# Optimization experiments

Measured on AMD Instinct MI355X. Metric: run time of the kernel, lower is better.

Reference implementation:

```python
import jax, jax.numpy as jnp
import numpy as np

EMBED_DIM = 1024
NUM_HEADS = 16
HEAD_DIM = EMBED_DIM // NUM_HEADS
MLP_HIDDEN = 4096


def layer_norm(x, gamma, beta, eps=1e-5):
    mu = jnp.mean(x, axis=-1, keepdims=True)
    var = jnp.var(x, axis=-1, keepdims=True)
    return (x - mu) / jnp.sqrt(var + eps) * gamma + beta


def setup_inputs() -> dict:
    key = jax.random.key(0)
    ks = jax.random.split(key, 16)
    d, h = EMBED_DIM, MLP_HIDDEN
    s = 0.02
    inp = {
        "x": jax.random.normal(ks[0], (2, 2048, d), dtype=jnp.float32),
        "ln1_g": jnp.ones((d,), jnp.float32),
        "ln1_b": jnp.zeros((d,), jnp.float32),
        "ln2_g": jnp.ones((d,), jnp.float32),
        "ln2_b": jnp.zeros((d,), jnp.float32),
        "Wq": jax.random.normal(ks[1], (d, d), jnp.float32) * s,
        "bq": jnp.zeros((d,), jnp.float32),
        "Wk": jax.random.normal(ks[2], (d, d), jnp.float32) * s,
        "bk": jnp.zeros((d,), jnp.float32),
        "Wv": jax.random.normal(ks[3], (d, d), jnp.float32) * s,
        "bv": jnp.zeros((d,), jnp.float32),
        "Wo": jax.random.normal(ks[4], (d, d), jnp.float32) * s,
        "bo": jnp.zeros((d,), jnp.float32),
        "W1": jax.random.normal(ks[5], (d, h), jnp.float32) * s,
        "b1": jnp.zeros((h,), jnp.float32),
        "W2": jax.random.normal(ks[6], (h, d), jnp.float32) * s,
        "b2": jnp.zeros((d,), jnp.float32),
    }
    return inp


def reference(x, ln1_g, ln1_b, ln2_g, ln2_b, Wq, bq, Wk, bk, Wv, bv, Wo, bo, W1, b1, W2, b2):
    B, T, C = x.shape
    H, Dh = NUM_HEADS, HEAD_DIM
    # attention branch
    xn = layer_norm(x, ln1_g, ln1_b)
    q = (xn @ Wq + bq).reshape(B, T, H, Dh).transpose(0, 2, 1, 3)  # [B,H,T,Dh]
    k = (xn @ Wk + bk).reshape(B, T, H, Dh).transpose(0, 2, 1, 3)
    v = (xn @ Wv + bv).reshape(B, T, H, Dh).transpose(0, 2, 1, 3)
    scores = jnp.einsum('bhtd,bhsd->bhts', q, k) / jnp.sqrt(jnp.float32(Dh))
    attn = jax.nn.softmax(scores, axis=-1)
    out = jnp.einsum('bhts,bhsd->bhtd', attn, v)
    out = out.transpose(0, 2, 1, 3).reshape(B, T, C)
    x = x + out @ Wo + bo
    # MLP branch
    xn2 = layer_norm(x, ln2_g, ln2_b)
    x = x + jax.nn.relu(xn2 @ W1 + b1) @ W2 + b2
    return x
```

## Files before the change

### kernel.cpp

```cpp
#include <hip/hip_runtime.h>

typedef float f32x4 __attribute__((ext_vector_type(4)));
typedef __bf16 bf16x8 __attribute__((ext_vector_type(8)));

constexpr int TT   = 2048;
constexpr int CC   = 1024;
constexpr int HIDN = 4096;
constexpr int MM   = 4096;
constexpr int NQKV = 3072;

union U84 { uint32_t u[4]; bf16x8 v; };

__device__ inline uint32_t cvt_pk_bf16(float lo, float hi) {
  uint32_t r;
  asm("v_cvt_pk_bf16_f32 %0, %1, %2" : "=v"(r) : "v"(lo), "v"(hi));
  return r;
}
__device__ inline ushort f2bf(float f) { return (ushort)(cvt_pk_bf16(f, 0.f) & 0xffffu); }
__device__ inline float bfbits2f(uint32_t bits) {
  union { uint32_t u; float f; } c; c.u = bits; return c.f;
}
__device__ inline float exp2_fast(float x) {
  float r;
  asm("v_exp_f32 %0, %1" : "=v"(r) : "v"(x));
  return r;
}

#define AS1C(p) ((__attribute__((address_space(1))) void*)(p))
#define AS3(p)  ((__attribute__((address_space(3))) void*)(p))

__global__ __launch_bounds__(256) void prep_weights(const float* __restrict__ Wq,
                                                    const float* __restrict__ Wk,
                                                    const float* __restrict__ Wv,
                                                    const float* __restrict__ Wo,
                                                    const float* __restrict__ W1,
                                                    const float* __restrict__ W2,
                                                    const float* __restrict__ bq,
                                                    const float* __restrict__ bk,
                                                    const float* __restrict__ bv,
                                                    const float* __restrict__ x,
                                                    const float* __restrict__ g1,
                                                    const float* __restrict__ b1v,
                                                    ushort* __restrict__ WqkvT,
                                                    ushort* __restrict__ WoT,
                                                    ushort* __restrict__ W1T,
                                                    ushort* __restrict__ W2T,
                                                    float* __restrict__ Bqkv,
                                                    ushort* __restrict__ Xn) {
  const int id = blockIdx.x;
  const int t = threadIdx.x;
  if (id >= 12300) {
    const int row = id - 12300;
    float4 v = reinterpret_cast<const float4*>(x + (size_t)row * CC)[t];
    float s  = v.x + v.y + v.z + v.w;
    float ss = v.x * v.x + v.y * v.y + v.z * v.z + v.w * v.w;
#pragma unroll
    for (int off = 32; off; off >>= 1) {
      s  += __shfl_down(s, off);
      ss += __shfl_down(ss, off);
    }
    __shared__ float red[16];
    const int wid = t >> 6, lane = t & 63;
    if (lane == 0) { red[wid] = s; red[8 + wid] = ss; }
    __syncthreads();
    if (t == 0) {
      red[0] = red[0] + red[1] + red[2] + red[3];
      red[8] = red[8] + red[9] + red[10] + red[11];
    }
    __syncthreads();
    const float mu   = red[0] * (1.0f / CC);
    const float var  = red[8] * (1.0f / CC) - mu * mu;
    const float rstd = rsqrtf(var + 1e-5f);
    float4 gg = reinterpret_cast<const float4*>(g1)[t];
    float4 bb = reinterpret_cast<const float4*>(b1v)[t];
    uint2 st;
    st.x = cvt_pk_bf16((v.x - mu) * rstd * gg.x + bb.x, (v.y - mu) * rstd * gg.y + bb.y);
    st.y = cvt_pk_bf16((v.z - mu) * rstd * gg.z + bb.z, (v.w - mu) * rstd * gg.w + bb.w);
    *reinterpret_cast<uint2*>(Xn + (size_t)row * CC + t * 4) = st;
    return;
  }
  if (id >= 12288) {
    const int i = (id - 12288) * 256 + t;
    Bqkv[i] = (i < 1024) ? bq[i] : ((i < 2048) ? bk[i - 1024] : bv[i - 2048]);
    return;
  }
  const float* W; ushort* out; int Kd, Nd, bx, by, rowOff = 0;
  if (id < 4096) {
    const int which = id >> 10, sub = id & 1023;
    bx = sub & 31; by = sub >> 5; Kd = 1024; Nd = 1024;
    if (which == 0)      { W = Wq; out = WqkvT; rowOff = 0; }
    else if (which == 1) { W = Wk; out = WqkvT; rowOff = 1024; }
    else if (which == 2) { W = Wv; out = WqkvT; rowOff = 2048; }
    else                 { W = Wo; out = WoT; }
  } else if (id < 8192) {
    const int sub = id - 4096; bx = sub & 127; by = sub >> 7;
    W = W1; out = W1T; Kd = 1024; Nd = 4096;
  } else {
    const int sub = id - 8192; bx = sub & 31; by = sub >> 5;
    W = W2; out = W2T; Kd = 4096; Nd = 1024;
  }
  const int n0 = bx * 32, k0 = by * 32;
  __shared__ float Ts[32][33];
  {
    const int r = t >> 3, cb = (t & 7) * 4;
    float4 v = *reinterpret_cast<const float4*>(W + (size_t)(k0 + r) * Nd + n0 + cb);
    Ts[r][cb + 0] = v.x; Ts[r][cb + 1] = v.y; Ts[r][cb + 2] = v.z; Ts[r][cb + 3] = v.w;
  }
  __syncthreads();
  {
    const int nl = t >> 3, kb = (t & 7) * 4;
    uint2 st;
    st.x = cvt_pk_bf16(Ts[kb + 0][nl], Ts[kb + 1][nl]);
    st.y = cvt_pk_bf16(Ts[kb + 2][nl], Ts[kb + 3][nl]);
    *reinterpret_cast<uint2*>(out + (size_t)(rowOff + n0 + nl) * Kd + k0 + kb) = st;
  }
}

template <bool RELU, bool VOUT, bool PARTIAL>
__global__ __launch_bounds__(512, 2) void gemm_8w(const ushort* __restrict__ A,
                                                  const ushort* __restrict__ Bt,
                                                  const float* __restrict__ bias,
                                                  ushort* __restrict__ outp,
                                                  ushort* __restrict__ Vt,
                                                  ushort* __restrict__ P1,
                                                  ushort* __restrict__ P2,
                                                  ushort* __restrict__ P3,
                                                  int N, int K, int Kchunk) {
  __shared__ ushort lds[65536];
  const int t = threadIdx.x, lane = t & 63, w = t >> 6;
  const int g = lane >> 4, i16 = lane & 15;
  const int wr = w >> 2, wc = w & 3;
  const int nwg  = gridDim.x * gridDim.y;
  const int orig = blockIdx.y * gridDim.x + blockIdx.x;
  const int sw   = (orig & 7) * (nwg >> 3) + (orig >> 3);
  const int row0 = (sw / gridDim.x) * 256, col0 = (sw % gridDim.x) * 256;
  const int kstart = PARTIAL ? blockIdx.z * Kchunk : 0;
  const int NT = (PARTIAL ? Kchunk : K) >> 6;
  ushort* __restrict__ Out = outp;
  if (PARTIAL) Out = (blockIdx.z == 0) ? outp : (blockIdx.z == 1) ? P1
              : (blockIdx.z == 2) ? P2 : P3;

  const ushort* aG[4];
  const ushort* bG[4];
#pragma unroll
  for (int i = 0; i < 4; ++i) {
    const int c = t + 512 * i;
    const int r = c >> 3, ssw = (c & 7) ^ (r & 7);
    aG[i] = A  + (size_t)(row0 + r) * K + kstart + ssw * 8;
    bG[i] = Bt + (size_t)(col0 + r) * K + kstart + ssw * 8;
  }

  int aoff[8][2], boff[4][2];
#pragma unroll
  for (int mf = 0; mf < 8; ++mf) {
    const int R = wr * 128 + mf * 16 + i16;
#pragma unroll
    for (int kk = 0; kk < 2; ++kk)
      aoff[mf][kk] = R * 128 + (((kk << 2) | g) ^ (R & 7)) * 16;
  }
#pragma unroll
  for (int nf = 0; nf < 4; ++nf) {
    const int Cn = wc * 64 + nf * 16 + i16;
#pragma unroll
    for (int kk = 0; kk < 2; ++kk)
      boff[nf][kk] = Cn * 128 + (((kk << 2) | g) ^ (Cn & 7)) * 16;
  }

  f32x4 acc[8][4] = {};

  auto STAGE = [&](int bi, int kt) {
    char* aB = (char*)lds + bi * 65536;
    char* bB = aB + 32768;
    const int ko = kt * 64;
#pragma unroll
    for (int i = 0; i < 4; ++i)
      __builtin_amdgcn_global_load_lds(AS1C(aG[i] + ko), AS3(aB + i * 8192 + w * 1024), 16, 0, 0);
#pragma unroll
    for (int i = 0; i < 4; ++i)
      __builtin_amdgcn_global_load_lds(AS1C(bG[i] + ko), AS3(bB + i * 8192 + w * 1024), 16, 0, 0);
  };

  STAGE(0, 0);

  for (int kt = 0; kt < NT; ++kt) {
    const int cur = kt & 1;
    if (kt + 1 < NT) {
      STAGE(cur ^ 1, kt + 1);
      asm volatile("s_waitcnt vmcnt(8)" ::: "memory");
    } else {
      asm volatile("s_waitcnt vmcnt(0)" ::: "memory");
    }
    asm volatile("s_barrier" ::: "memory");
    __builtin_amdgcn_sched_barrier(0);

    const char* aB = (const char*)lds + cur * 65536;
    const char* bB = aB + 32768;
    bf16x8 b4[4][2], a4[4][2];
#pragma unroll
    for (int nf = 0; nf < 4; ++nf)
#pragma unroll
      for (int kk = 0; kk < 2; ++kk)
        b4[nf][kk] = *reinterpret_cast<const bf16x8*>(bB + boff[nf][kk]);
#pragma unroll
    for (int mf = 0; mf < 4; ++mf)
#pragma unroll
      for (int kk = 0; kk < 2; ++kk)
        a4[mf][kk] = *reinterpret_cast<const bf16x8*>(aB + aoff[mf][kk]);
    __builtin_amdgcn_s_setprio(1);
#pragma unroll
    for (int mf = 0; mf < 4; ++mf)
#pragma unroll
      for (int nf = 0; nf < 4; ++nf)
#pragma unroll
        for (int kk = 0; kk < 2; ++kk)
          acc[mf][nf] = __builtin_amdgcn_mfma_f32_16x16x32_bf16(a4[mf][kk], b4[nf][kk], acc[mf][nf], 0, 0, 0);
    __builtin_amdgcn_s_setprio(0);
    asm volatile("s_barrier" ::: "memory");
    __builtin_amdgcn_sched_barrier(0);
#pragma unroll
    for (int mf = 0; mf < 4; ++mf)
#pragma unroll
      for (int kk = 0; kk < 2; ++kk)
        a4[mf][kk] = *reinterpret_cast<const bf16x8*>(aB + aoff[mf + 4][kk]);
    __builtin_amdgcn_s_setprio(1);
#pragma unroll
    for (int mf = 0; mf < 4; ++mf)
#pragma unroll
      for (int nf = 0; nf < 4; ++nf)
#pragma unroll
        for (int kk = 0; kk < 2; ++kk)
          acc[mf + 4][nf] = __builtin_amdgcn_mfma_f32_16x16x32_bf16(a4[mf][kk], b4[nf][kk], acc[mf + 4][nf], 0, 0, 0);
    __builtin_amdgcn_s_setprio(0);
    asm volatile("s_barrier" ::: "memory");
    __builtin_amdgcn_sched_barrier(0);
  }

  const int qcol0 = col0 + wc * 64;

  if (VOUT && qcol0 >= 2048) {
#pragma unroll
    for (int nf = 0; nf < 4; ++nf) {
      const int ncol = qcol0 + nf * 16 + i16;
      const float bb = bias[ncol];
      const int d = ncol - 2048;
      const int hh = d >> 6, dd = d & 63;
#pragma unroll
      for (int mf = 0; mf < 8; ++mf) {
        const int mrow = row0 + wr * 128 + mf * 16 + 4 * g;
        const int bb_ = mrow >> 11, tok = mrow & 2047;
        uint2 st;
        st.x = cvt_pk_bf16(acc[mf][nf][0] + bb, acc[mf][nf][1] + bb);
        st.y = cvt_pk_bf16(acc[mf][nf][2] + bb, acc[mf][nf][3] + bb);
        *reinterpret_cast<uint2*>(Vt + (size_t)((bb_ * 16 + hh) * 64 + dd) * TT + tok) = st;
      }
    }
    return;
  }

  float* Lf = (float*)((char*)lds + w * 4096);
  const int rr2 = lane >> 2, q = lane & 3;
#pragma unroll
  for (int mf = 0; mf < 8; ++mf) {
#pragma unroll
    for (int nf = 0; nf < 4; ++nf)
#pragma unroll
      for (int r = 0; r < 4; ++r) {
        const int row = 4 * g + r;
        Lf[row * 64 + ((16 * nf + i16) ^ ((row & 7) << 2))] = acc[mf][nf][r];
      }
    asm volatile("s_waitcnt lgkmcnt(0)" ::: "memory");
    uint32_t u[8];
#pragma unroll
    for (int j = 0; j < 4; ++j) {
      f32x4 v = *reinterpret_cast<const f32x4*>(Lf + rr2 * 64 + ((q * 16 + 4 * j) ^ ((rr2 & 7) << 2)));
      float e0 = v[0], e1 = v[1], e2 = v[2], e3 = v[3];
      if (!PARTIAL) {
        const float4 b4v = *reinterpret_cast<const float4*>(bias + qcol0 + q * 16 + 4 * j);
        e0 += b4v.x; e1 += b4v.y; e2 += b4v.z; e3 += b4v.w;
        if (RELU) {
          e0 = fmaxf(e0, 0.f); e1 = fmaxf(e1, 0.f);
          e2 = fmaxf(e2, 0.f); e3 = fmaxf(e3, 0.f);
        }
      }
      u[2 * j + 0] = cvt_pk_bf16(e0, e1);
      u[2 * j + 1] = cvt_pk_bf16(e2, e3);
    }
    const int mrow = row0 + wr * 128 + mf * 16 + rr2;
    ushort* orow = Out + (size_t)mrow * N + qcol0 + q * 16;
    uint4 s0; s0.x = u[0]; s0.y = u[1]; s0.z = u[2]; s0.w = u[3];
    uint4 s1; s1.x = u[4]; s1.y = u[5]; s1.z = u[6]; s1.w = u[7];
    *reinterpret_cast<uint4*>(orow) = s0;
    *reinterpret_cast<uint4*>(orow + 8) = s1;
    asm volatile("s_waitcnt lgkmcnt(0)" ::: "memory");
  }
}

__device__ inline float bfsum4(uint32_t a, uint32_t b, uint32_t c, uint32_t d, bool hi) {
  if (hi) return bfbits2f(a & 0xffff0000u) + bfbits2f(b & 0xffff0000u) +
                 bfbits2f(c & 0xffff0000u) + bfbits2f(d & 0xffff0000u);
  return bfbits2f(a << 16) + bfbits2f(b << 16) + bfbits2f(c << 16) + bfbits2f(d << 16);
}

__global__ __launch_bounds__(256) void reduce_wo_ln(const ushort* __restrict__ P0,
                                                    const ushort* __restrict__ P1,
                                                    const ushort* __restrict__ P2,
                                                    const ushort* __restrict__ P3,
                                                    const float* __restrict__ x,
                                                    const float* __restrict__ bo,
                                                    const float* __restrict__ g,
                                                    const float* __restrict__ b,
                                                    float* __restrict__ X1f,
                                                    ushort* __restrict__ Xn) {
  const int row = blockIdx.x, t = threadIdx.x;
  const size_t off = (size_t)row * CC + t * 4;
  float4 v  = *reinterpret_cast<const float4*>(x + off);
  const uint2 q0 = *reinterpret_cast<const uint2*>(P0 + off);
  const uint2 q1 = *reinterpret_cast<const uint2*>(P1 + off);
  const uint2 q2 = *reinterpret_cast<const uint2*>(P2 + off);
  const uint2 q3 = *reinterpret_cast<const uint2*>(P3 + off);
  float4 bb = reinterpret_cast<const float4*>(bo)[t];
  v.x += bfsum4(q0.x, q1.x, q2.x, q3.x, false) + bb.x;
  v.y += bfsum4(q0.x, q1.x, q2.x, q3.x, true)  + bb.y;
  v.z += bfsum4(q0.y, q1.y, q2.y, q3.y, false) + bb.z;
  v.w += bfsum4(q0.y, q1.y, q2.y, q3.y, true)  + bb.w;
  *reinterpret_cast<float4*>(X1f + off) = v;

  float s  = v.x + v.y + v.z + v.w;
  float ss = v.x * v.x + v.y * v.y + v.z * v.z + v.w * v.w;
#pragma unroll
  for (int o = 32; o; o >>= 1) {
    s  += __shfl_down(s, o);
    ss += __shfl_down(ss, o);
  }
  __shared__ float red[16];
  const int wid = t >> 6, lane = t & 63;
  if (lane == 0) { red[wid] = s; red[8 + wid] = ss; }
  __syncthreads();
  if (t == 0) {
    red[0] = red[0] + red[1] + red[2] + red[3];
    red[8] = red[8] + red[9] + red[10] + red[11];
  }
  __syncthreads();
  const float mu   = red[0] * (1.0f / CC);
  const float var  = red[8] * (1.0f / CC) - mu * mu;
  const float rstd = rsqrtf(var + 1e-5f);
  float4 gg = reinterpret_cast<const float4*>(g)[t];
  float4 lb = reinterpret_cast<const float4*>(b)[t];
  uint2 st;
  st.x = cvt_pk_bf16((v.x - mu) * rstd * gg.x + lb.x, (v.y - mu) * rstd * gg.y + lb.y);
  st.y = cvt_pk_bf16((v.z - mu) * rstd * gg.z + lb.z, (v.w - mu) * rstd * gg.w + lb.w);
  *reinterpret_cast<uint2*>(Xn + off) = st;
}

__global__ __launch_bounds__(256) void reduce_fc2(const ushort* __restrict__ P0,
                                                  const ushort* __restrict__ P1,
                                                  const ushort* __restrict__ P2,
                                                  const ushort* __restrict__ P3,
                                                  const float* __restrict__ X1,
                                                  const float* __restrict__ b2,
                                                  float* __restrict__ out) {
  const int row = blockIdx.x, t = threadIdx.x;
  const size_t off = (size_t)row * CC + t * 4;
  float4 v  = *reinterpret_cast<const float4*>(X1 + off);
  const uint2 q0 = *reinterpret_cast<const uint2*>(P0 + off);
  const uint2 q1 = *reinterpret_cast<const uint2*>(P1 + off);
  const uint2 q2 = *reinterpret_cast<const uint2*>(P2 + off);
  const uint2 q3 = *reinterpret_cast<const uint2*>(P3 + off);
  float4 bb = reinterpret_cast<const float4*>(b2)[t];
  v.x += bfsum4(q0.x, q1.x, q2.x, q3.x, false) + bb.x;
  v.y += bfsum4(q0.x, q1.x, q2.x, q3.x, true)  + bb.y;
  v.z += bfsum4(q0.y, q1.y, q2.y, q3.y, false) + bb.z;
  v.w += bfsum4(q0.y, q1.y, q2.y, q3.y, true)  + bb.w;
  *reinterpret_cast<float4*>(out + off) = v;
}

__global__ __launch_bounds__(512, 4) void attn_partial(const ushort* __restrict__ qkv,
                                                       const ushort* __restrict__ Vt,
                                                       ushort* __restrict__ O0,
                                                       ushort* __restrict__ O1,
                                                       float* __restrict__ lbuf) {
  __shared__ ushort Ks[2][4096];
  __shared__ ushort Vs[2][4096];
  __shared__ uint32_t Ps[8][16][36];
  const int t = threadIdx.x, lane = t & 63, w = t >> 6;
  const int g = lane >> 4, iq = lane & 15;
  const int flat = blockIdx.x;
  const int work = (flat & 7) * 128 + (flat >> 3);
  const int bh = work >> 5;
  const int rem = work & 31;
  const int z = rem >> 4;
  const int qt = rem & 15;
  const int b = bh >> 4, h = bh & 15;
  ushort* __restrict__ Obuf = z ? O1 : O0;

  bf16x8 qfrag[2];
  {
    const ushort* qrow = qkv + (size_t)(b * TT + qt * 128 + w * 16 + iq) * NQKV + h * 64;
    const float qs = 0.125f * 1.44269504f;
#pragma unroll
    for (int kk = 0; kk < 2; ++kk) {
      uint4 raw = *reinterpret_cast<const uint4*>(qrow + kk * 32 + g * 8);
      uint32_t rr[4] = {raw.x, raw.y, raw.z, raw.w};
      U84 tmp;
#pragma unroll
      for (int c = 0; c < 4; ++c) {
        float lo = bfbits2f(rr[c] << 16) * qs;
        float hi = bfbits2f(rr[c] & 0xffff0000u) * qs;
        tmp.u[c] = cvt_pk_bf16(lo, hi);
      }
      qfrag[kk] = tmp.v;
    }
  }

  const int sr1 = t >> 3, sc1 = t & 7;
  const int csw = (sc1 ^ (sr1 & 7)) * 8;
  const ushort* kbase = qkv + 1024 + h * 64;
  const ushort* vbase = Vt + (size_t)(bh * 64) * TT;

  auto STAGE = [&](int bi, int kt) {
    const size_t tok = (size_t)(b * TT + kt * 64);
    __builtin_amdgcn_global_load_lds(AS1C(kbase + (tok + sr1) * NQKV + csw),
                                     AS3((char*)&Ks[bi][0] + w * 1024), 16, 0, 0);
    __builtin_amdgcn_global_load_lds(AS1C(vbase + (size_t)sr1 * TT + kt * 64 + csw),
                                     AS3((char*)&Vs[bi][0] + w * 1024), 16, 0, 0);
  };

  uint32_t (*pw)[36] = Ps[w];
  const int wsw = (iq & 8) << 1;
  const int xsb = wsw << 2;
  const char* prow = (const char*)&pw[iq][0];

  float lrun = 0.f;
  f32x4 ot[4] = {};

  const int kt0 = z * 16, ktE = kt0 + 16;
  STAGE(0, kt0);

  for (int kt = kt0; kt < ktE; ++kt) {
    const int cur = kt & 1;
    if (kt + 1 < ktE) {
      STAGE(cur ^ 1, kt + 1);
      asm volatile("s_waitcnt vmcnt(2)" ::: "memory");
    } else {
      asm volatile("s_waitcnt vmcnt(0)" ::: "memory");
    }
    asm volatile("s_barrier" ::: "memory");
    __builtin_amdgcn_sched_barrier(0);
    const char* Kc = (const char*)&Ks[cur][0];
    const char* Vc = (const char*)&Vs[cur][0];

    f32x4 sfr[4] = {};
    __builtin_amdgcn_s_setprio(1);
#pragma unroll
    for (int kk = 0; kk < 2; ++kk)
#pragma unroll
      for (int jf = 0; jf < 4; ++jf) {
        const int row = iq + 16 * jf;
        const int off = row * 128 + ((kk * 64 + g * 16) ^ ((row & 7) << 4));
        bf16x8 a = *reinterpret_cast<const bf16x8*>(Kc + off);
        sfr[jf] = __builtin_amdgcn_mfma_f32_16x16x32_bf16(a, qfrag[kk], sfr[jf], 0, 0, 0);
      }
    __builtin_amdgcn_s_setprio(0);

#pragma unroll
    for (int f = 0; f < 4; ++f) {
      float p0 = exp2_fast(sfr[f][0]);
      float p1 = exp2_fast(sfr[f][1]);
      float p2 = exp2_fast(sfr[f][2]);
      float p3 = exp2_fast(sfr[f][3]);
      lrun += (p0 + p1) + (p2 + p3);
      uint2 st2;
      st2.x = cvt_pk_bf16(p0, p1);
      st2.y = cvt_pk_bf16(p2, p3);
      *reinterpret_cast<uint2*>(&pw[iq][(8 * f + 2 * g) ^ wsw]) = st2;
    }
    asm volatile("s_waitcnt lgkmcnt(0)" ::: "memory");

    __builtin_amdgcn_s_setprio(1);
#pragma unroll
    for (int kk = 0; kk < 2; ++kk) {
      bf16x8 pb = *reinterpret_cast<const bf16x8*>(prow + ((kk * 64 + g * 16) ^ xsb));
#pragma unroll
      for (int df = 0; df < 4; ++df) {
        const int row = iq + 16 * df;
        const int off = row * 128 + ((kk * 64 + g * 16) ^ ((row & 7) << 4));
        bf16x8 a = *reinterpret_cast<const bf16x8*>(Vc + off);
        ot[df] = __builtin_amdgcn_mfma_f32_16x16x32_bf16(a, pb, ot[df], 0, 0, 0);
      }
    }
    __builtin_amdgcn_s_setprio(0);

    asm volatile("s_barrier" ::: "memory");
    __builtin_amdgcn_sched_barrier(0);
  }

  lrun += __shfl_xor(lrun, 16, 64);
  lrun += __shfl_xor(lrun, 32, 64);
  const int grow = b * TT + qt * 128 + w * 16 + iq;
  ushort* orow = Obuf + (size_t)grow * CC + h * 64;
#pragma unroll
  for (int df = 0; df < 4; ++df) {
    uint2 st;
    st.x = cvt_pk_bf16(ot[df][0], ot[df][1]);
    st.y = cvt_pk_bf16(ot[df][2], ot[df][3]);
    *reinterpret_cast<uint2*>(orow + df * 16 + g * 4) = st;
  }
  if (g == 0 && (lane >> 4) == 0)
    lbuf[(size_t)z * (MM * 16) + (size_t)grow * 16 + h] = lrun;
}

__global__ __launch_bounds__(256) void attn_combine(const ushort* __restrict__ O0,
                                                    const ushort* __restrict__ O1,
                                                    const float* __restrict__ lbuf,
                                                    ushort* __restrict__ attnb) {
  const int row = blockIdx.x, t = threadIdx.x;
  const int h = t >> 4;
  const float l0 = lbuf[(size_t)row * 16 + h];
  const float l1 = lbuf[(size_t)MM * 16 + (size_t)row * 16 + h];
  const float inv = 1.f / (l0 + l1);
  const size_t off = (size_t)row * CC + t * 4;
  const uint2 r0 = *reinterpret_cast<const uint2*>(O0 + off);
  const uint2 r1 = *reinterpret_cast<const uint2*>(O1 + off);
  const float o0 = (bfbits2f(r0.x << 16)         + bfbits2f(r1.x << 16))         * inv;
  const float o1 = (bfbits2f(r0.x & 0xffff0000u) + bfbits2f(r1.x & 0xffff0000u)) * inv;
  const float o2 = (bfbits2f(r0.y << 16)         + bfbits2f(r1.y << 16))         * inv;
  const float o3 = (bfbits2f(r0.y & 0xffff0000u) + bfbits2f(r1.y & 0xffff0000u)) * inv;
  uint2 st;
  st.x = cvt_pk_bf16(o0, o1);
  st.y = cvt_pk_bf16(o2, o3);
  *reinterpret_cast<uint2*>(attnb + off) = st;
}

extern "C" void kernel_launch(void* const* d_in, const int* in_sizes, int n_in,
                              void* d_out, int out_size, void* d_ws, size_t ws_size,
                              hipStream_t stream) {
  const float* x     = (const float*)d_in[0];
  const float* ln1_g = (const float*)d_in[1];
  const float* ln1_b = (const float*)d_in[2];
  const float* ln2_g = (const float*)d_in[3];
  const float* ln2_b = (const float*)d_in[4];
  const float* Wq = (const float*)d_in[5];
  const float* bq = (const float*)d_in[6];
  const float* Wk = (const float*)d_in[7];
  const float* bk = (const float*)d_in[8];
  const float* Wv = (const float*)d_in[9];
  const float* bv = (const float*)d_in[10];
  const float* Wo = (const float*)d_in[11];
  const float* bo = (const float*)d_in[12];
  const float* W1 = (const float*)d_in[13];
  const float* b1 = (const float*)d_in[14];
  const float* W2 = (const float*)d_in[15];
  const float* b2 = (const float*)d_in[16];
  float* out = (float*)d_out;
  char* ws = (char*)d_ws;

  ushort* WqkvT = (ushort*)(ws + 0);
  ushort* WoT   = (ushort*)(ws + 6291456);
  ushort* W1T   = (ushort*)(ws + 8388608);
  ushort* W2T   = (ushort*)(ws + 16777216);
  float*  Bqkv  = (float*) (ws + 25165824);
  ushort* Xn    = (ushort*)(ws + 25178112);
  ushort* Attn  = (ushort*)(ws + 33566720);
  float*  X1f   = (float*) (ws + 41955328);
  ushort* Qkv   = (ushort*)(ws + 58732544);
  ushort* Vtb   = (ushort*)(ws + 83898368);
  ushort* Hid   = (ushort*)(ws + 58732544);
  ushort* OP0   = (ushort*)(ws + 41955328);
  ushort* OP1   = (ushort*)(ws + 50343936);
  float*  lbuf  = (float*) (ws + 0);
  ushort* WoP0  = (ushort*)(ws + 58732544);
  ushort* WoP1  = (ushort*)(ws + 67121152);
  ushort* WoP2  = (ushort*)(ws + 75509760);
  ushort* WoP3  = (ushort*)(ws + 83898368);
  ushort* F2P0  = (ushort*)(ws + 0);
  ushort* F2P1  = (ushort*)(ws + 8388608);
  ushort* F2P2  = (ushort*)(ws + 25178112);
  ushort* F2P3  = (ushort*)(ws + 33566720);

  const dim3 blk(256);

  prep_weights<<<dim3(16396), blk, 0, stream>>>(Wq, Wk, Wv, Wo, W1, W2, bq, bk, bv,
                                                x, ln1_g, ln1_b,
                                                WqkvT, WoT, W1T, W2T, Bqkv, Xn);
  gemm_8w<false, true, false><<<dim3(12, 16), dim3(512), 0, stream>>>(
      Xn, WqkvT, Bqkv, Qkv, Vtb, nullptr, nullptr, nullptr, NQKV, 1024, 0);
  attn_partial<<<dim3(1024), dim3(512), 0, stream>>>(Qkv, Vtb, OP0, OP1, lbuf);
  attn_combine<<<dim3(MM), blk, 0, stream>>>(OP0, OP1, lbuf, Attn);
  gemm_8w<false, false, true><<<dim3(4, 16, 4), dim3(512), 0, stream>>>(
      Attn, WoT, nullptr, WoP0, nullptr, WoP1, WoP2, WoP3, 1024, 1024, 256);
  reduce_wo_ln<<<dim3(MM), blk, 0, stream>>>(WoP0, WoP1, WoP2, WoP3, x, bo, ln2_g, ln2_b, X1f, Xn);
  gemm_8w<true, false, false><<<dim3(16, 16), dim3(512), 0, stream>>>(
      Xn, W1T, b1, Hid, nullptr, nullptr, nullptr, nullptr, HIDN, 1024, 0);
  gemm_8w<false, false, true><<<dim3(4, 16, 4), dim3(512), 0, stream>>>(
      Hid, W2T, nullptr, F2P0, nullptr, F2P1, F2P2, F2P3, 1024, 4096, 1024);
  reduce_fc2<<<dim3(MM), blk, 0, stream>>>(F2P0, F2P1, F2P2, F2P3, X1f, b2, out);
}
```

Before: 236.1 us.

## Drop split-KV attention and combine kernel; normalize inside single attention pass

Removes the two-way key split in attention so each block processes the full key range and normalizes its output by the row sum before storing. This eliminates the attn_combine kernel launch and the round trip of the partial outputs and row sums through global memory. The cost is half as many blocks (512 instead of 1024) with twice the loop length each, which lowers parallelism and may leave compute units underfilled on a large GPU.

Result: faster. 227.0 us (median of 2 runs) (-3.9%).

```diff
diff --git a/kernel.cpp b/kernel.cpp
--- a/kernel.cpp
+++ b/kernel.cpp
@@ -374,24 +374,19 @@
   *reinterpret_cast<float4*>(out + off) = v;
 }
 
-__global__ __launch_bounds__(512, 4) void attn_partial(const ushort* __restrict__ qkv,
-                                                       const ushort* __restrict__ Vt,
-                                                       ushort* __restrict__ O0,
-                                                       ushort* __restrict__ O1,
-                                                       float* __restrict__ lbuf) {
+__global__ __launch_bounds__(512, 4) void attn_full(const ushort* __restrict__ qkv,
+                                                    const ushort* __restrict__ Vt,
+                                                    ushort* __restrict__ attnb) {
   __shared__ ushort Ks[2][4096];
   __shared__ ushort Vs[2][4096];
   __shared__ uint32_t Ps[8][16][36];
   const int t = threadIdx.x, lane = t & 63, w = t >> 6;
   const int g = lane >> 4, iq = lane & 15;
   const int flat = blockIdx.x;
-  const int work = (flat & 7) * 128 + (flat >> 3);
-  const int bh = work >> 5;
-  const int rem = work & 31;
-  const int z = rem >> 4;
-  const int qt = rem & 15;
+  const int work = (flat & 7) * 64 + (flat >> 3);
+  const int bh = work >> 4;
+  const int qt = work & 15;
   const int b = bh >> 4, h = bh & 15;
-  ushort* __restrict__ Obuf = z ? O1 : O0;
 
   bf16x8 qfrag[2];
   {
@@ -433,12 +428,12 @@
   float lrun = 0.f;
   f32x4 ot[4] = {};
 
-  const int kt0 = z * 16, ktE = kt0 + 16;
-  STAGE(0, kt0);
-
-  for (int kt = kt0; kt < ktE; ++kt) {
+  constexpr int NKT = TT / 64;
+  STAGE(0, 0);
+
+  for (int kt = 0; kt < NKT; ++kt) {
     const int cur = kt & 1;
-    if (kt + 1 < ktE) {
+    if (kt + 1 < NKT) {
       STAGE(cur ^ 1, kt + 1);
       asm volatile("s_waitcnt vmcnt(2)" ::: "memory");
     } else {
@@ -497,38 +492,15 @@
   lrun += __shfl_xor(lrun, 16, 64);
   lrun += __shfl_xor(lrun, 32, 64);
   const int grow = b * TT + qt * 128 + w * 16 + iq;
-  ushort* orow = Obuf + (size_t)grow * CC + h * 64;
+  const float inv = 1.f / lrun;
+  ushort* orow = attnb + (size_t)grow * CC + h * 64;
 #pragma unroll
   for (int df = 0; df < 4; ++df) {
     uint2 st;
-    st.x = cvt_pk_bf16(ot[df][0], ot[df][1]);
-    st.y = cvt_pk_bf16(ot[df][2], ot[df][3]);
+    st.x = cvt_pk_bf16(ot[df][0] * inv, ot[df][1] * inv);
+    st.y = cvt_pk_bf16(ot[df][2] * inv, ot[df][3] * inv);
     *reinterpret_cast<uint2*>(orow + df * 16 + g * 4) = st;
   }
-  if (g == 0 && (lane >> 4) == 0)
-    lbuf[(size_t)z * (MM * 16) + (size_t)grow * 16 + h] = lrun;
-}
-
-__global__ __launch_bounds__(256) void attn_combine(const ushort* __restrict__ O0,
-                                                    const ushort* __restrict__ O1,
-                                                    const float* __restrict__ lbuf,
-                                                    ushort* __restrict__ attnb) {
-  const int row = blockIdx.x, t = threadIdx.x;
-  const int h = t >> 4;
-  const float l0 = lbuf[(size_t)row * 16 + h];
-  const float l1 = lbuf[(size_t)MM * 16 + (size_t)row * 16 + h];
-  const float inv = 1.f / (l0 + l1);
-  const size_t off = (size_t)row * CC + t * 4;
-  const uint2 r0 = *reinterpret_cast<const uint2*>(O0 + off);
-  const uint2 r1 = *reinterpret_cast<const uint2*>(O1 + off);
-  const float o0 = (bfbits2f(r0.x << 16)         + bfbits2f(r1.x << 16))         * inv;
-  const float o1 = (bfbits2f(r0.x & 0xffff0000u) + bfbits2f(r1.x & 0xffff0000u)) * inv;
-  const float o2 = (bfbits2f(r0.y << 16)         + bfbits2f(r1.y << 16))         * inv;
-  const float o3 = (bfbits2f(r0.y & 0xffff0000u) + bfbits2f(r1.y & 0xffff0000u)) * inv;
-  uint2 st;
-  st.x = cvt_pk_bf16(o0, o1);
-  st.y = cvt_pk_bf16(o2, o3);
-  *reinterpret_cast<uint2*>(attnb + off) = st;
 }
 
 extern "C" void kernel_launch(void* const* d_in, const int* in_sizes, int n_in,
@@ -565,9 +537,6 @@
   ushort* Qkv   = (ushort*)(ws + 58732544);
   ushort* Vtb   = (ushort*)(ws + 83898368);
   ushort* Hid   = (ushort*)(ws + 58732544);
-  ushort* OP0   = (ushort*)(ws + 41955328);
-  ushort* OP1   = (ushort*)(ws + 50343936);
-  float*  lbuf  = (float*) (ws + 0);
   ushort* WoP0  = (ushort*)(ws + 58732544);
   ushort* WoP1  = (ushort*)(ws + 67121152);
   ushort* WoP2  = (ushort*)(ws + 75509760);
@@ -584,8 +553,7 @@
                                                 WqkvT, WoT, W1T, W2T, Bqkv, Xn);
   gemm_8w<false, true, false><<<dim3(12, 16), dim3(512), 0, stream>>>(
       Xn, WqkvT, Bqkv, Qkv, Vtb, nullptr, nullptr, nullptr, NQKV, 1024, 0);
-  attn_partial<<<dim3(1024), dim3(512), 0, stream>>>(Qkv, Vtb, OP0, OP1, lbuf);
-  attn_combine<<<dim3(MM), blk, 0, stream>>>(OP0, OP1, lbuf, Attn);
+  attn_full<<<dim3(512), dim3(512), 0, stream>>>(Qkv, Vtb, Attn);
   gemm_8w<false, false, true><<<dim3(4, 16, 4), dim3(512), 0, stream>>>(
       Attn, WoT, nullptr, WoP0, nullptr, WoP1, WoP2, WoP3, 1024, 1024, 256);
   reduce_wo_ln<<<dim3(MM), blk, 0, stream>>>(WoP0, WoP1, WoP2, WoP3, x, bo, ln2_g, ln2_b, X1f, Xn);
```
